# Performance work log

Measured on AMD Instinct MI355X. Metric: run time of the kernel, lower is better.

The kernel has to match this reference:

```python
import jax, jax.numpy as jnp
from jax import lax
import numpy as np

# Quantization / layer config (mirrors QuantizedConv2d init_kwargs)
IN_ZP = 3
OUT_ZP = -2
IN_SCALE = 0.05
OUT_SCALE = 0.1
STRIDE = (1, 1)
PAD = (1, 1)  # (pad_h, pad_w)
DILATION = (1, 1)
GROUPS = 1
FEATURE_BITS = 8
Q_MIN, Q_MAX = -(1 << (FEATURE_BITS - 1)), (1 << (FEATURE_BITS - 1)) - 1  # -128, 127


def setup_inputs() -> dict:
    key = jax.random.key(0)
    k1, k2, k3, k4 = jax.random.split(key, 4)
    N, Cin, H, W = 32, 128, 56, 56
    Cout, KH, KW = 256, 3, 3
    x = jax.random.randint(k1, (N, Cin, H, W), -128, 128, dtype=jnp.int8)
    weight = jax.random.randint(k2, (Cout, Cin, KH, KW), -128, 128, dtype=jnp.int8)
    bias = jax.random.randint(k3, (Cout,), -1000, 1000, dtype=jnp.int32)  # shifted quantized bias
    weight_scale = jax.random.uniform(k4, (Cout,), dtype=jnp.float32, minval=1e-3, maxval=1e-2)
    return {"x": x, "weight": weight, "bias": bias, "weight_scale": weight_scale}


def reference(x, weight, bias, weight_scale):
    # q_y = round((CONV[q_x, q_w] + shifted_bias) * (S_x * S_w / S_y) + Z_y), clamped to int8
    # Pad with the input zero point (NOT zero), matching F.pad(..., value=input_zero_point)
    ph, pw = PAD
    xp = jnp.pad(x, ((0, 0), (0, 0), (ph, ph), (pw, pw)), constant_values=IN_ZP)
    # Exact integer convolution (matches the CPU int32 path; GPU float path rounds
    # back to the same int32 values)
    acc = lax.conv_general_dilated(
        xp.astype(jnp.int32), weight.astype(jnp.int32),
        window_strides=STRIDE, padding='VALID',
        rhs_dilation=DILATION, feature_group_count=GROUPS,
        dimension_numbers=('NCHW', 'OIHW', 'NCHW'))  # [N, Cout, H, W] int32
    acc = acc + bias[None, :, None, None]
    # Fused dequant/requant epilogue: per-channel scale, output zero point, round, clamp
    scale = (IN_SCALE * weight_scale / OUT_SCALE)[None, :, None, None]  # [1, Cout, 1, 1]
    y = acc.astype(jnp.float32) * scale + jnp.float32(OUT_ZP)
    return jnp.clip(jnp.round(y), Q_MIN, Q_MAX).astype(jnp.int8)
```

## Files before the change

### kernel.cpp

```cpp
#include <hip/hip_runtime.h>


#define NB    32
#define CIN   128
#define HH    56
#define WW    56
#define COUT  256
#define HP    58
#define WP    58
#define PIX   (HH*WW)
#define KTOT  1152
#define NCHUNK 18

#define NPT   28
#define BN    112
#define NJ    7
#define BBYTES (NJ*1024)

typedef int v4i __attribute__((ext_vector_type(4)));

#define GLOAD_LDS(gsrc, ldst) \
    __builtin_amdgcn_global_load_lds( \
        (const __attribute__((address_space(1))) void*)(gsrc), \
        (__attribute__((address_space(3))) void*)(ldst), 16, 0, 0)

__global__ void pack_x_kernel(const int* __restrict__ x,
                              unsigned char* __restrict__ xp8,
                              int n0) {
    int bx = blockIdx.x;
    int nl = bx / HP;
    int hp = bx % HP;
    int nb = n0 + nl;
    int tid = threadIdx.x;
    unsigned int* rowo = (unsigned int*)(xp8 + (size_t)(nl*HP + hp) * WP * CIN);

    if (hp == 0 || hp == HP-1) {
        const v4i zp = {0x03030303, 0x03030303, 0x03030303, 0x03030303};
        for (int i = tid; i < (WP*CIN)/16; i += 256)
            ((v4i*)rowo)[i] = zp;
        return;
    }

    __shared__ unsigned int lt[WW * 33];

    int h  = hp - 1;
    int wl = tid & 63;
    int cg = tid >> 6;
    if (wl < WW) {
        const int s = HH*WW;
#pragma unroll
        for (int k = 0; k < 8; ++k) {
            int ci0 = cg*4 + k*16;
            const int* xb = x + (((size_t)(nb*CIN + ci0)*HH + h)*WW + wl);
            int v0 = xb[0], v1 = xb[s], v2 = xb[2*s], v3 = xb[3*s];
            unsigned int pack = (v0 & 0xFF) | ((v1 & 0xFF) << 8) |
                                ((v2 & 0xFF) << 16) | ((unsigned)(v3 & 0xFF) << 24);
            lt[wl*33 + (ci0 >> 2)] = pack;
        }
    }
    __syncthreads();

#pragma unroll
    for (int it = 0; it < 7; ++it) {
        int idx = it*256 + tid;
        int p = idx >> 5;
        int d = idx & 31;
        rowo[(p + 1)*32 + d] = lt[p*33 + d];
    }
    if (tid < 64) {
        int off = (tid < 32) ? tid : ((WP-1)*32 + (tid - 32));
        rowo[off] = 0x03030303u;
    }
}

__global__ void pack_w_kernel(const int* __restrict__ wt,
                              unsigned char* __restrict__ w8f) {
    int co = blockIdx.x;
    int t  = threadIdx.x;
    for (int idx = t; idx < KTOT/4; idx += 128) {
        int k  = idx * 4;
        int r  = k >> 7;
        int ci = k & 127;
        const int* wb = wt + ((co*CIN + ci)*9 + r);
        int v0 = wb[0], v1 = wb[9], v2 = wb[18], v3 = wb[27];
        unsigned int pack = (v0 & 0xFF) | ((v1 & 0xFF) << 8) |
                            ((v2 & 0xFF) << 16) | ((unsigned)(v3 & 0xFF) << 24);
        int tch = k >> 6;
        size_t dst = ((size_t)((tch*16 + (co >> 4))*16 + (co & 15)))*64 + (k & 63);
        *(unsigned int*)(w8f + dst) = pack;
    }
}

__device__ __forceinline__ int koff_of(int t) {
    int r  = t >> 1;
    int kh = (r >= 6) ? 2 : (r >= 3 ? 1 : 0);
    int kw = r - kh*3;
    return ((kh*WP + kw) << 7) + ((t & 1) << 6);
}

__launch_bounds__(256, 2)
__global__ void conv_kernel(const unsigned char* __restrict__ w8f,
                            const unsigned char* __restrict__ xp8,
                            const int* __restrict__ bias,
                            const float* __restrict__ wscale,
                            int* __restrict__ out,
                            int n0) {
    __shared__ __align__(16) unsigned char ldsB[2*BBYTES];

    int bx = blockIdx.x;
    int pt = bx % NPT;
    int nl = bx / NPT;
    int nb = n0 + nl;
    int p0 = pt * BN;

    int tid  = threadIdx.x;
    int lane = tid & 63;
    int wm   = tid >> 6;
    int lr   = lane & 15;
    int lg   = lane >> 4;

    int l4 = lane >> 2;
    int sw = (lane & 3) ^ ((lane >> 3) & 3);
    int s0 = wm*2;
    int s1 = (wm*2+1 > 6) ? 6 : wm*2+1;
    int s0u = __builtin_amdgcn_readfirstlane(s0);
    int s1u = __builtin_amdgcn_readfirstlane(s1);
    int pA = p0 + s0*16 + l4;
    int pB = p0 + s1*16 + l4;
    const unsigned char* bsrc0 =
        xp8 + ((size_t)((nl*HP + pA/WW)*WP + pA%WW))*CIN + sw*16;
    const unsigned char* bsrc1 =
        xp8 + ((size_t)((nl*HP + pB/WW)*WP + pB%WW))*CIN + sw*16;

    int rslot = lg ^ ((lr >> 1) & 3);
    int vb = lr*64 + rslot*16;

    const unsigned char* abase = w8f + (size_t)(wm*4)*1024 + (lr*64 + lg*16);

    v4i acc[4][NJ];
#pragma unroll
    for (int i = 0; i < 4; ++i)
#pragma unroll
        for (int j = 0; j < NJ; ++j)
            acc[i][j] = (v4i){0, 0, 0, 0};

#define STAGE_B(T, BUFOFF) do {                                                \
        int koff_ = koff_of(T);                                                \
        GLOAD_LDS(bsrc0 + koff_, &ldsB[(BUFOFF) + s0u*1024]);                  \
        GLOAD_LDS(bsrc1 + koff_, &ldsB[(BUFOFF) + s1u*1024]);                  \
    } while (0)

    v4i a_cur[4], a_nxt[4];
    STAGE_B(0, 0);
#pragma unroll
    for (int i = 0; i < 4; ++i) a_cur[i] = *(const v4i*)(abase + i*1024);

#pragma unroll
    for (int t = 0; t < NCHUNK; ++t) {
        if (t < NCHUNK-1) {
            STAGE_B(t+1, ((t+1)&1)*BBYTES);
#pragma unroll
            for (int i = 0; i < 4; ++i)
                a_nxt[i] = *(const v4i*)(abase + (size_t)(t+1)*16384 + i*1024);
            asm volatile("s_waitcnt vmcnt(10)" ::: "memory");
        } else {
            asm volatile("s_waitcnt vmcnt(4)" ::: "memory");
        }
        __builtin_amdgcn_sched_barrier(0);
        __builtin_amdgcn_s_barrier();

        v4i b_[NJ];
#pragma unroll
        for (int j = 0; j < NJ; ++j)
            b_[j] = *(const v4i*)&ldsB[(t&1)*BBYTES + vb + j*1024];
#pragma unroll
        for (int i = 0; i < 4; ++i)
#pragma unroll
            for (int j = 0; j < NJ; ++j)
                acc[i][j] = __builtin_amdgcn_mfma_i32_16x16x64_i8(
                    a_cur[i], b_[j], acc[i][j], 0, 0, 0);

        __builtin_amdgcn_s_barrier();
        if (t < NCHUNK-1) {
#pragma unroll
            for (int i = 0; i < 4; ++i) a_cur[i] = a_nxt[i];
        }
    }
#undef STAGE_B

#pragma unroll
    for (int i = 0; i < 4; ++i) {
#pragma unroll
        for (int rr = 0; rr < 4; ++rr) {
            int co = wm*64 + i*16 + lg*4 + rr;
            float sc = __fdiv_rn(__fmul_rn(0.05f, wscale[co]), 0.1f);
            int bs = bias[co];
            int* orow = out + ((size_t)(nb*COUT + co))*PIX + p0;
#pragma unroll
            for (int j = 0; j < NJ; ++j) {
                float accf = (float)(acc[i][j][rr] + bs);
                float y = __fadd_rn(__fmul_rn(accf, sc), -2.0f);
                y = rintf(y);
                y = fminf(fmaxf(y, -128.0f), 127.0f);
                orow[j*16 + lr] = (int)y;
            }
        }
    }
}

__launch_bounds__(256)
__global__ void conv_direct_kernel(const int* __restrict__ x,
                                   const int* __restrict__ wt,
                                   const int* __restrict__ bias,
                                   const float* __restrict__ wscale,
                                   int* __restrict__ out) {
    size_t idx = (size_t)blockIdx.x * 256 + threadIdx.x;
    if (idx >= (size_t)NB * COUT * PIX) return;
    int w  = idx % WW;
    int h  = (idx / WW) % HH;
    int co = (idx / PIX) % COUT;
    int nb = idx / ((size_t)PIX * COUT);
    int acc = 0;
    for (int ci = 0; ci < CIN; ++ci) {
        const int* xb = x + ((size_t)(nb*CIN + ci)*HH)*WW;
        const int* wb = wt + ((size_t)(co*CIN + ci)*9);
        for (int kh = 0; kh < 3; ++kh) {
            int hh = h + kh - 1;
            for (int kw = 0; kw < 3; ++kw) {
                int ww2 = w + kw - 1;
                int xv = (hh >= 0 && hh < HH && ww2 >= 0 && ww2 < WW)
                         ? xb[hh*WW + ww2] : 3;
                acc += xv * wb[kh*3 + kw];
            }
        }
    }
    float sc = __fdiv_rn(__fmul_rn(0.05f, wscale[co]), 0.1f);
    float y = __fadd_rn(__fmul_rn((float)(acc + bias[co]), sc), -2.0f);
    y = rintf(y);
    y = fminf(fmaxf(y, -128.0f), 127.0f);
    out[idx] = (int)y;
}

extern "C" void kernel_launch(void* const* d_in, const int* in_sizes, int n_in,
                              void* d_out, int out_size, void* d_ws, size_t ws_size,
                              hipStream_t stream) {
    const int*   x      = (const int*)d_in[0];
    const int*   weight = (const int*)d_in[1];
    const int*   bias   = (const int*)d_in[2];
    const float* wscale = (const float*)d_in[3];
    int*         out    = (int*)d_out;

    const size_t XOFF = 320u << 10;
    const size_t BPB  = (size_t)HP * WP * CIN;

    int nchk = 0;
    if (ws_size >= XOFF + BPB) {
        size_t navail = (ws_size - XOFF) / BPB;
        nchk = navail >= 32 ? 32 : navail >= 16 ? 16 : navail >= 8 ? 8
             : navail >= 4 ? 4 : navail >= 2 ? 2 : 1;
    }

    if (nchk == 0) {
        size_t total = (size_t)NB * COUT * PIX;
        conv_direct_kernel<<<dim3((total + 255) / 256), dim3(256), 0, stream>>>(
            x, weight, bias, wscale, out);
        return;
    }

    unsigned char* ws  = (unsigned char*)d_ws;
    unsigned char* w8f = ws;
    unsigned char* xp8 = ws + XOFF;

    pack_w_kernel<<<dim3(COUT), dim3(128), 0, stream>>>(weight, w8f);
    for (int n0 = 0; n0 < NB; n0 += nchk) {
        int nc = (NB - n0 < nchk) ? (NB - n0) : nchk;
        pack_x_kernel<<<dim3(nc*HP), dim3(256), 0, stream>>>(x, xp8, n0);
        conv_kernel<<<dim3(NPT*nc), dim3(256), 0, stream>>>(w8f, xp8, bias, wscale, out, n0);
    }
}
```

Before: 63.72 us.

## Fuse input packing into conv kernel with per-block LDS halo tile

Removes the separate pack_x kernel and padded int8 workspace. Each conv block now loads its four-row input halo straight from the int32 input, packs it to int8 with the zero-point border into swizzled LDS, and reads all 18 K-chunks from that resident tile. Per-chunk double-buffered global-to-LDS staging and the barriers around it go away. The cost is that overlapping halo rows are re-read from global by neighbouring blocks, there is a serial load phase before any MFMA work, and LDS use grows, which may affect occupancy.

```diff
diff --git a/kernel.cpp b/kernel.cpp
--- a/kernel.cpp
+++ b/kernel.cpp
@@ -6,8 +6,6 @@
 #define HH    56
 #define WW    56
 #define COUT  256
-#define HP    58
-#define WP    58
 #define PIX   (HH*WW)
 #define KTOT  1152
 #define NCHUNK 18
@@ -15,63 +13,10 @@
 #define NPT   28
 #define BN    112
 #define NJ    7
-#define BBYTES (NJ*1024)
+#define IMGC  58
+#define IMGB  (4*IMGC*128)
 
 typedef int v4i __attribute__((ext_vector_type(4)));
-
-#define GLOAD_LDS(gsrc, ldst) \
-    __builtin_amdgcn_global_load_lds( \
-        (const __attribute__((address_space(1))) void*)(gsrc), \
-        (__attribute__((address_space(3))) void*)(ldst), 16, 0, 0)
-
-__global__ void pack_x_kernel(const int* __restrict__ x,
-                              unsigned char* __restrict__ xp8,
-                              int n0) {
-    int bx = blockIdx.x;
-    int nl = bx / HP;
-    int hp = bx % HP;
-    int nb = n0 + nl;
-    int tid = threadIdx.x;
-    unsigned int* rowo = (unsigned int*)(xp8 + (size_t)(nl*HP + hp) * WP * CIN);
-
-    if (hp == 0 || hp == HP-1) {
-        const v4i zp = {0x03030303, 0x03030303, 0x03030303, 0x03030303};
-        for (int i = tid; i < (WP*CIN)/16; i += 256)
-            ((v4i*)rowo)[i] = zp;
-        return;
-    }
-
-    __shared__ unsigned int lt[WW * 33];
-
-    int h  = hp - 1;
-    int wl = tid & 63;
-    int cg = tid >> 6;
-    if (wl < WW) {
-        const int s = HH*WW;
-#pragma unroll
-        for (int k = 0; k < 8; ++k) {
-            int ci0 = cg*4 + k*16;
-            const int* xb = x + (((size_t)(nb*CIN + ci0)*HH + h)*WW + wl);
-            int v0 = xb[0], v1 = xb[s], v2 = xb[2*s], v3 = xb[3*s];
-            unsigned int pack = (v0 & 0xFF) | ((v1 & 0xFF) << 8) |
-                                ((v2 & 0xFF) << 16) | ((unsigned)(v3 & 0xFF) << 24);
-            lt[wl*33 + (ci0 >> 2)] = pack;
-        }
-    }
-    __syncthreads();
-
-#pragma unroll
-    for (int it = 0; it < 7; ++it) {
-        int idx = it*256 + tid;
-        int p = idx >> 5;
-        int d = idx & 31;
-        rowo[(p + 1)*32 + d] = lt[p*33 + d];
-    }
-    if (tid < 64) {
-        int off = (tid < 32) ? tid : ((WP-1)*32 + (tid - 32));
-        rowo[off] = 0x03030303u;
-    }
-}
 
 __global__ void pack_w_kernel(const int* __restrict__ wt,
                               unsigned char* __restrict__ w8f) {
@@ -91,26 +36,18 @@
     }
 }
 
-__device__ __forceinline__ int koff_of(int t) {
-    int r  = t >> 1;
-    int kh = (r >= 6) ? 2 : (r >= 3 ? 1 : 0);
-    int kw = r - kh*3;
-    return ((kh*WP + kw) << 7) + ((t & 1) << 6);
-}
-
 __launch_bounds__(256, 2)
 __global__ void conv_kernel(const unsigned char* __restrict__ w8f,
-                            const unsigned char* __restrict__ xp8,
+                            const int* __restrict__ x,
                             const int* __restrict__ bias,
                             const float* __restrict__ wscale,
-                            int* __restrict__ out,
-                            int n0) {
-    __shared__ __align__(16) unsigned char ldsB[2*BBYTES];
+                            int* __restrict__ out) {
+    __shared__ __align__(16) unsigned char img[IMGB];
 
     int bx = blockIdx.x;
     int pt = bx % NPT;
-    int nl = bx / NPT;
-    int nb = n0 + nl;
+    int nb = bx / NPT;
+    int h0 = pt * 2;
     int p0 = pt * BN;
 
     int tid  = threadIdx.x;
@@ -119,21 +56,49 @@
     int lr   = lane & 15;
     int lg   = lane >> 4;
 
-    int l4 = lane >> 2;
-    int sw = (lane & 3) ^ ((lane >> 3) & 3);
-    int s0 = wm*2;
-    int s1 = (wm*2+1 > 6) ? 6 : wm*2+1;
-    int s0u = __builtin_amdgcn_readfirstlane(s0);
-    int s1u = __builtin_amdgcn_readfirstlane(s1);
-    int pA = p0 + s0*16 + l4;
-    int pB = p0 + s1*16 + l4;
-    const unsigned char* bsrc0 =
-        xp8 + ((size_t)((nl*HP + pA/WW)*WP + pA%WW))*CIN + sw*16;
-    const unsigned char* bsrc1 =
-        xp8 + ((size_t)((nl*HP + pB/WW)*WP + pB%WW))*CIN + sw*16;
-
-    int rslot = lg ^ ((lr >> 1) & 3);
-    int vb = lr*64 + rslot*16;
+    {
+        int wl = lane;
+        int cg = wm;
+        const int s = HH*WW;
+#pragma unroll
+        for (int hh = 0; hh < 4; ++hh) {
+            int hi = h0 - 1 + hh;
+            unsigned int* rowl = (unsigned int*)&img[hh*IMGC*128];
+            if (hi < 0 || hi >= HH) {
+                for (int i = tid; i < IMGC*32; i += 256)
+                    rowl[i] = 0x03030303u;
+            } else {
+                if (tid < 64) {
+                    int off = (tid < 32) ? tid : (57*32 + (tid - 32));
+                    rowl[off] = 0x03030303u;
+                }
+                if (wl < WW) {
+#pragma unroll
+                    for (int k = 0; k < 8; ++k) {
+                        int ci0 = cg*4 + k*16;
+                        const int* xb = x + (((size_t)(nb*CIN + ci0)*HH + hi)*WW + wl);
+                        int v0 = xb[0], v1 = xb[s], v2 = xb[2*s], v3 = xb[3*s];
+                        unsigned int pack = (v0 & 0xFF) | ((v1 & 0xFF) << 8) |
+                                            ((v2 & 0xFF) << 16) |
+                                            ((unsigned)(v3 & 0xFF) << 24);
+                        int waddr = ((hh*IMGC + wl + 1) << 7) + ci0;
+                        waddr ^= ((waddr >> 7) & 7) << 4;
+                        *(unsigned int*)&img[waddr] = pack;
+                    }
+                }
+            }
+        }
+    }
+    __syncthreads();
+
+    int pre[NJ];
+#pragma unroll
+    for (int j = 0; j < NJ; ++j) {
+        int p = j*16 + lr;
+        int r = (p >= 56) ? 1 : 0;
+        int c = p - 56*r;
+        pre[j] = (r*IMGC + c) << 7;
+    }
 
     const unsigned char* abase = w8f + (size_t)(wm*4)*1024 + (lr*64 + lg*16);
 
@@ -144,49 +109,40 @@
         for (int j = 0; j < NJ; ++j)
             acc[i][j] = (v4i){0, 0, 0, 0};
 
-#define STAGE_B(T, BUFOFF) do {                                                \
-        int koff_ = koff_of(T);                                                \
-        GLOAD_LDS(bsrc0 + koff_, &ldsB[(BUFOFF) + s0u*1024]);                  \
-        GLOAD_LDS(bsrc1 + koff_, &ldsB[(BUFOFF) + s1u*1024]);                  \
-    } while (0)
-
     v4i a_cur[4], a_nxt[4];
-    STAGE_B(0, 0);
 #pragma unroll
     for (int i = 0; i < 4; ++i) a_cur[i] = *(const v4i*)(abase + i*1024);
 
 #pragma unroll
     for (int t = 0; t < NCHUNK; ++t) {
         if (t < NCHUNK-1) {
-            STAGE_B(t+1, ((t+1)&1)*BBYTES);
 #pragma unroll
             for (int i = 0; i < 4; ++i)
                 a_nxt[i] = *(const v4i*)(abase + (size_t)(t+1)*16384 + i*1024);
-            asm volatile("s_waitcnt vmcnt(10)" ::: "memory");
-        } else {
-            asm volatile("s_waitcnt vmcnt(4)" ::: "memory");
-        }
-        __builtin_amdgcn_sched_barrier(0);
-        __builtin_amdgcn_s_barrier();
+        }
+        int r  = t >> 1;
+        int kh = (r >= 6) ? 2 : (r >= 3 ? 1 : 0);
+        int kw = r - kh*3;
+        int uoff = ((kh*IMGC + kw) << 7) + ((t & 1) << 6) + lg*16;
 
         v4i b_[NJ];
 #pragma unroll
-        for (int j = 0; j < NJ; ++j)
-            b_[j] = *(const v4i*)&ldsB[(t&1)*BBYTES + vb + j*1024];
+        for (int j = 0; j < NJ; ++j) {
+            int ba = pre[j] + uoff;
+            ba ^= ((ba >> 7) & 7) << 4;
+            b_[j] = *(const v4i*)&img[ba];
+        }
 #pragma unroll
         for (int i = 0; i < 4; ++i)
 #pragma unroll
             for (int j = 0; j < NJ; ++j)
                 acc[i][j] = __builtin_amdgcn_mfma_i32_16x16x64_i8(
                     a_cur[i], b_[j], acc[i][j], 0, 0, 0);
-
-        __builtin_amdgcn_s_barrier();
         if (t < NCHUNK-1) {
 #pragma unroll
             for (int i = 0; i < 4; ++i) a_cur[i] = a_nxt[i];
         }
     }
-#undef STAGE_B
 
 #pragma unroll
     for (int i = 0; i < 4; ++i) {
@@ -250,31 +206,14 @@
     const float* wscale = (const float*)d_in[3];
     int*         out    = (int*)d_out;
 
-    const size_t XOFF = 320u << 10;
-    const size_t BPB  = (size_t)HP * WP * CIN;
-
-    int nchk = 0;
-    if (ws_size >= XOFF + BPB) {
-        size_t navail = (ws_size - XOFF) / BPB;
-        nchk = navail >= 32 ? 32 : navail >= 16 ? 16 : navail >= 8 ? 8
-             : navail >= 4 ? 4 : navail >= 2 ? 2 : 1;
-    }
-
-    if (nchk == 0) {
+    if (ws_size < 294912) {
         size_t total = (size_t)NB * COUT * PIX;
         conv_direct_kernel<<<dim3((total + 255) / 256), dim3(256), 0, stream>>>(
             x, weight, bias, wscale, out);
         return;
     }
 
-    unsigned char* ws  = (unsigned char*)d_ws;
-    unsigned char* w8f = ws;
-    unsigned char* xp8 = ws + XOFF;
-
+    unsigned char* w8f = (unsigned char*)d_ws;
     pack_w_kernel<<<dim3(COUT), dim3(128), 0, stream>>>(weight, w8f);
-    for (int n0 = 0; n0 < NB; n0 += nchk) {
-        int nc = (NB - n0 < nchk) ? (NB - n0) : nchk;
-        pack_x_kernel<<<dim3(nc*HP), dim3(256), 0, stream>>>(x, xp8, n0);
-        conv_kernel<<<dim3(NPT*nc), dim3(256), 0, stream>>>(w8f, xp8, bias, wscale, out, n0);
-    }
-}
+    conv_kernel<<<dim3(NPT*NB), dim3(256), 0, stream>>>(w8f, x, bias, wscale, out);
+}
```

Measured after the change: 82.09 us. 28.8% more time.

## Triple-buffer B tiles in LDS with two K-chunks per barrier phase

Applied to the files above, without the earlier changes.

Restructures the main loop so each phase stages two K-chunks of the input tile into one of three LDS buffers. Each phase then needs a single barrier instead of two barriers per chunk. Weight fragments for both chunks are loaded directly in the phase instead of being prefetched a chunk ahead. This is meant to cut barrier and synchronization overhead and deepen the B prefetch. The cost is three times more LDS, and weight-load latency may now be exposed before the MFMAs.

```diff
diff --git a/kernel.cpp b/kernel.cpp
--- a/kernel.cpp
+++ b/kernel.cpp
@@ -11,11 +11,13 @@
 #define PIX   (HH*WW)
 #define KTOT  1152
 #define NCHUNK 18
+#define NPHASE 9
 
 #define NPT   28
 #define BN    112
 #define NJ    7
-#define BBYTES (NJ*1024)
+#define CHB   (NJ*1024)
+#define PHB   (2*CHB)
 
 typedef int v4i __attribute__((ext_vector_type(4)));
 
@@ -105,7 +107,7 @@
                             const float* __restrict__ wscale,
                             int* __restrict__ out,
                             int n0) {
-    __shared__ __align__(16) unsigned char ldsB[2*BBYTES];
+    __shared__ __align__(16) unsigned char ldsB[3*PHB];
 
     int bx = blockIdx.x;
     int pt = bx % NPT;
@@ -144,49 +146,54 @@
         for (int j = 0; j < NJ; ++j)
             acc[i][j] = (v4i){0, 0, 0, 0};
 
-#define STAGE_B(T, BUFOFF) do {                                                \
-        int koff_ = koff_of(T);                                                \
-        GLOAD_LDS(bsrc0 + koff_, &ldsB[(BUFOFF) + s0u*1024]);                  \
-        GLOAD_LDS(bsrc1 + koff_, &ldsB[(BUFOFF) + s1u*1024]);                  \
+#define STAGE2(P, ROFF) do {                                                   \
+        int k0_ = koff_of(2*(P));                                              \
+        int k1_ = koff_of(2*(P)+1);                                            \
+        GLOAD_LDS(bsrc0 + k0_, &ldsB[(ROFF) + s0u*1024]);                      \
+        GLOAD_LDS(bsrc1 + k0_, &ldsB[(ROFF) + s1u*1024]);                      \
+        GLOAD_LDS(bsrc0 + k1_, &ldsB[(ROFF) + CHB + s0u*1024]);                \
+        GLOAD_LDS(bsrc1 + k1_, &ldsB[(ROFF) + CHB + s1u*1024]);                \
     } while (0)
 
-    v4i a_cur[4], a_nxt[4];
-    STAGE_B(0, 0);
-#pragma unroll
-    for (int i = 0; i < 4; ++i) a_cur[i] = *(const v4i*)(abase + i*1024);
-
-#pragma unroll
-    for (int t = 0; t < NCHUNK; ++t) {
-        if (t < NCHUNK-1) {
-            STAGE_B(t+1, ((t+1)&1)*BBYTES);
-#pragma unroll
-            for (int i = 0; i < 4; ++i)
-                a_nxt[i] = *(const v4i*)(abase + (size_t)(t+1)*16384 + i*1024);
-            asm volatile("s_waitcnt vmcnt(10)" ::: "memory");
-        } else {
-            asm volatile("s_waitcnt vmcnt(4)" ::: "memory");
-        }
+    STAGE2(0, 0);
+
+#pragma unroll
+    for (int p = 0; p < NPHASE; ++p) {
+        if (p < NPHASE-1) STAGE2(p+1, ((p+1)%3)*PHB);
+
+        v4i a_[8];
+#pragma unroll
+        for (int i = 0; i < 4; ++i) {
+            a_[i]   = *(const v4i*)(abase + (size_t)(2*p)*16384   + i*1024);
+            a_[4+i] = *(const v4i*)(abase + (size_t)(2*p+1)*16384 + i*1024);
+        }
+
+        asm volatile("s_waitcnt vmcnt(12)" ::: "memory");
         __builtin_amdgcn_sched_barrier(0);
         __builtin_amdgcn_s_barrier();
 
+        int roff = (p % 3) * PHB;
         v4i b_[NJ];
 #pragma unroll
         for (int j = 0; j < NJ; ++j)
-            b_[j] = *(const v4i*)&ldsB[(t&1)*BBYTES + vb + j*1024];
+            b_[j] = *(const v4i*)&ldsB[roff + vb + j*1024];
 #pragma unroll
         for (int i = 0; i < 4; ++i)
 #pragma unroll
             for (int j = 0; j < NJ; ++j)
                 acc[i][j] = __builtin_amdgcn_mfma_i32_16x16x64_i8(
-                    a_cur[i], b_[j], acc[i][j], 0, 0, 0);
-
-        __builtin_amdgcn_s_barrier();
-        if (t < NCHUNK-1) {
-#pragma unroll
-            for (int i = 0; i < 4; ++i) a_cur[i] = a_nxt[i];
-        }
-    }
-#undef STAGE_B
+                    a_[i], b_[j], acc[i][j], 0, 0, 0);
+#pragma unroll
+        for (int j = 0; j < NJ; ++j)
+            b_[j] = *(const v4i*)&ldsB[roff + CHB + vb + j*1024];
+#pragma unroll
+        for (int i = 0; i < 4; ++i)
+#pragma unroll
+            for (int j = 0; j < NJ; ++j)
+                acc[i][j] = __builtin_amdgcn_mfma_i32_16x16x64_i8(
+                    a_[4+i], b_[j], acc[i][j], 0, 0, 0);
+    }
+#undef STAGE2
 
 #pragma unroll
     for (int i = 0; i < 4; ++i) {
```

After: 63.59 us. No clear change (-0.2%).
